# Kernel tuning notes

Hardware: AMD Instinct MI355X
Metric: run time of the kernel (lower is better)

The kernel has to match this reference:

```python
import jax, jax.numpy as jnp
import numpy as np

B, T, C, H = 4, 4096, 384, 64

def setup_inputs() -> dict:
    key = jax.random.key(0)
    ks = jax.random.split(key, 7)
    return {
        "x": jax.random.normal(ks[0], (B, T, C), dtype=jnp.float32),
        "Wk": jax.random.normal(ks[1], (H, C), dtype=jnp.float32) * 0.05,
        "bk": jax.random.normal(ks[2], (H,), dtype=jnp.float32) * 0.05,
        "Wq": jax.random.normal(ks[3], (H, C), dtype=jnp.float32) * 0.05,
        "bq": jax.random.normal(ks[4], (H,), dtype=jnp.float32) * 0.05,
        "Wv": jax.random.normal(ks[5], (H, C), dtype=jnp.float32) * 0.05,
        "bv": jax.random.normal(ks[6], (H,), dtype=jnp.float32) * 0.05,
    }

def reference(x, Wk, bk, Wq, bq, Wv, bv):
    # Faithful to the source, including its quirks:
    #   - q = self.value(x)   (query uses the VALUE projection; Wq/bq unused)
    #   - scale = C ** -0.5 with C = embedding dim (384), not head dim
    #   - dropout in eval mode (identity)
    Bb, Tt, Cc = x.shape
    k = x @ Wk.T + bk                                  # (B,T,H)
    q = x @ Wv.T + bv                                  # (B,T,H)  <- bug reproduced
    scale = jnp.float32(Cc) ** -0.5
    scores = jnp.einsum('bth,bsh->bts', q, k) * scale  # (B,T,T)
    mask = jnp.tril(jnp.ones((Tt, Tt), dtype=bool))    # causal mask
    scores = jnp.where(mask, scores, jnp.float32(-jnp.inf))
    w = jax.nn.softmax(scores, axis=-1)                # (B,T,T)
    v = x @ Wv.T + bv                                  # (B,T,H)
    return jnp.einsum('bts,bsh->bth', w, v)            # (B,T,H)
```

## Files before the change

kernel.cpp:

```cpp
#include <hip/hip_runtime.h>

#define T_SEQ 4096
#define CDIM 384

typedef __attribute__((ext_vector_type(8))) short short8;
typedef __attribute__((ext_vector_type(4))) short short4e;
typedef __attribute__((ext_vector_type(4))) float float4e;

#define KSCALE 0.05103103630798288f
#define KE (KSCALE * 1.4426950408889634f)

__device__ inline unsigned short f2bf(float f) {
  unsigned u = __builtin_bit_cast(unsigned, f);
  u += 0x7FFFu + ((u >> 16) & 1u);
  return (unsigned short)(u >> 16);
}

__device__ inline void dma16(const void* g, void* l) {
  __builtin_amdgcn_global_load_lds(
      (const __attribute__((address_space(1))) unsigned int*)g,
      (__attribute__((address_space(3))) unsigned int*)l, 16, 0, 0);
}

__global__ __launch_bounds__(256) void proj_kernel(
    const float* __restrict__ x, const float* __restrict__ Wk, const float* __restrict__ bk,
    const float* __restrict__ Wv, const float* __restrict__ bv,
    unsigned short* __restrict__ Ktil, unsigned short* __restrict__ Qrow,
    unsigned short* __restrict__ Vtil) {
  __shared__ alignas(16) char plds[24576];
  unsigned short (*Wl)[5120] = (unsigned short (*)[5120])plds;
  const int tid = threadIdx.x;
  const int lane = tid & 63;
  const int w = tid >> 6;
  const int lid = lane & 15, quad = lane >> 4;
  const int blockRow0 = blockIdx.x * 64;
  const float* xr = x + (size_t)(blockRow0 + w * 16 + lid) * CDIM;

  float4e wreg[4];
  int wcol[4], wpart[4];
#pragma unroll
  for (int i = 0; i < 4; i++) {
    const int f = tid + 256 * i;
    wcol[i] = f >> 3; wpart[i] = f & 7;
  }
  auto wload = [&](int kc) {
#pragma unroll
    for (int i = 0; i < 4; i++) {
      const float* wsrc = (wcol[i] < 64)
          ? (Wk + (size_t)wcol[i] * CDIM + kc * 32 + wpart[i] * 4)
          : (Wv + (size_t)(wcol[i] - 64) * CDIM + kc * 32 + wpart[i] * 4);
      wreg[i] = *(const float4e*)wsrc;
    }
  };
  auto wstage = [&](int bufi) {
#pragma unroll
    for (int i = 0; i < 4; i++) {
      short4e s;
#pragma unroll
      for (int jj = 0; jj < 4; jj++) s[jj] = (short)f2bf(wreg[i][jj]);
      *(short4e*)(&Wl[bufi][wcol[i] * 40 + wpart[i] * 4]) = s;
    }
  };
  float4e xa0[2], xa1[2];
  auto xload = [&](int kc, int slot) {
    xa0[slot] = *(const float4e*)(xr + kc * 32 + quad * 8);
    xa1[slot] = *(const float4e*)(xr + kc * 32 + quad * 8 + 4);
  };

  wload(0); wstage(0);
  wload(1);
  xload(0, 0); xload(1, 1);
  __syncthreads();

  float4e acc[8];
#pragma unroll
  for (int n = 0; n < 8; n++) acc[n] = (float4e){0.f, 0.f, 0.f, 0.f};

  for (int kc = 0; kc < 12; kc++) {
    if (kc < 11) wstage((kc + 1) & 1);
    if (kc < 10) wload(kc + 2);
    const int slot = kc & 1;
    short8 af;
#pragma unroll
    for (int jj = 0; jj < 4; jj++) {
      af[jj] = (short)f2bf(xa0[slot][jj]);
      af[4 + jj] = (short)f2bf(xa1[slot][jj]);
    }
    if (kc < 10) xload(kc + 2, slot);
#pragma unroll
    for (int n = 0; n < 8; n++) {
      short8 bf = *(const short8*)(&Wl[kc & 1][(n * 16 + lid) * 40 + quad * 8]);
      acc[n] = __builtin_amdgcn_mfma_f32_16x16x32_bf16(af, bf, acc[n], 0, 0, 0);
    }
    __syncthreads();
  }

  unsigned short* Sl = (unsigned short*)plds;
  const int b = blockRow0 >> 12;
  const int kt32 = (blockRow0 & 4095) >> 5;
  const int sec = w >> 1;
  const int kob = (w & 1) * 16 + quad * 4;
#pragma unroll
  for (int n = 0; n < 8; n++) {
    const int col = n * 16 + lid;
    const float bias = (n < 4) ? bk[col] : bv[col - 64];
#pragma unroll
    for (int i = 0; i < 4; i++) {
      const int ko = kob + i;
      const float val = acc[n][i] + bias;
      if (n < 4) {
        Sl[sec * 6144 + ko * 64 + (((col >> 3) ^ (ko & 7)) * 8) + (col & 7)] = f2bf(val);
      } else {
        const int hh = col - 64;
        Sl[sec * 6144 + 4096 + ko * 64 + hh] = f2bf(val * KE);
        Sl[sec * 6144 + 2048 + hh * 32 + (((ko >> 3) ^ ((hh >> 1) & 3)) * 8) + (ko & 7)] = f2bf(val);
      }
    }
  }
  __syncthreads();
#pragma unroll
  for (int s = 0; s < 2; s++) {
    const size_t tile = (size_t)(b * 128 + kt32 + s) * 2048;
    *(short8*)(Ktil + tile + tid * 8) = *(const short8*)(&Sl[s * 6144 + tid * 8]);
    *(short8*)(Vtil + tile + tid * 8) = *(const short8*)(&Sl[s * 6144 + 2048 + tid * 8]);
  }
#pragma unroll
  for (int r = 0; r < 2; r++) {
    const int slot = tid + r * 256;
    const int s2 = slot >> 8, off = slot & 255;
    *(short8*)(Qrow + (size_t)blockRow0 * 64 + slot * 8) =
        *(const short8*)(&Sl[s2 * 6144 + 4096 + off * 8]);
  }
}

__global__ __launch_bounds__(256, 2) void attn_kernel(
    const unsigned short* __restrict__ Ktil, const unsigned short* __restrict__ Qrow,
    const unsigned short* __restrict__ Vtil,
    float* __restrict__ Opart, float* __restrict__ MLpart,
    int segT, int maxseg, int segshift) {
  __shared__ alignas(16) char lds[51200];
  const int j = blockIdx.x;
  const int b = j & 3;
  const int rest = j >> 2;
  const int qb = 31 - (rest >> segshift);
  const int seg = rest & (maxseg - 1);
  const int t0 = seg * segT;
  const int tendb = 2 * qb + 2;
  if (t0 >= tendb) return;
  const int tend = (t0 + segT < tendb) ? t0 + segT : tendb;

  const int wv = threadIdx.x >> 6;
  const int lane = threadIdx.x & 63;
  const int lid = lane & 15, quad = lane >> 4;
  const int qt = qb * 4 + wv;
  const int q0 = qt * 32;
  const int tcap = qt >> 1;

  const unsigned short* Qb = Qrow + (size_t)(b * T_SEQ + q0) * 64;
  const char* Kg = (const char*)(Ktil + (size_t)(b * 128) * 2048);
  const char* Vg = (const char*)(Vtil + (size_t)(b * 128) * 2048);
  char* Pbase = lds + 32768 + wv * 4608;

  short8 Qf[2][2];
#pragma unroll
  for (int qq = 0; qq < 2; qq++)
#pragma unroll
    for (int h = 0; h < 2; h++)
      Qf[qq][h] = *(const short8*)(Qb + (size_t)(qq * 16 + lid) * 64 + h * 32 + quad * 8);

  float4e Ot[2][4];
  float lrow[2] = {0.f, 0.f};
#pragma unroll
  for (int qq = 0; qq < 2; qq++)
#pragma unroll
    for (int cc = 0; cc < 4; cc++) Ot[qq][cc] = (float4e){0.f, 0.f, 0.f, 0.f};
  const float4e zero4 = (float4e){0.f, 0.f, 0.f, 0.f};

  auto stage = [&](int t, int bufi) {
#pragma unroll
    for (int c = 0; c < 4; c++) {
      const int o = wv * 4 + c;
      const char* src = (o < 8) ? (Kg + (size_t)t * 8192 + o * 1024)
                                : (Vg + (size_t)t * 8192 + (o - 8) * 1024);
      char* dst = (o < 8) ? (lds + bufi * 8192 + o * 1024)
                          : (lds + 16384 + bufi * 8192 + (o - 8) * 1024);
      dma16(src + lane * 16, dst);
    }
  };

  stage(t0, 0);
  __asm__ __volatile__("s_waitcnt vmcnt(0)" ::: "memory");
  __syncthreads();

  for (int t = t0; t < tend; t++) {
    const int cb = (t - t0) & 1, nb = cb ^ 1;
    if (t + 1 < tend) stage(t + 1, nb);

    if (t <= tcap) {
      const int k0 = t * 64;
#pragma unroll
      for (int ksub = 0; ksub < 2; ksub++) {
        short8 Kf[2][2];
#pragma unroll
        for (int kb2 = 0; kb2 < 2; kb2++) {
          const int row32 = kb2 * 16 + lid;
#pragma unroll
          for (int h = 0; h < 2; h++) {
            const int gran = (h * 4 + quad) ^ (row32 & 7);
            Kf[kb2][h] = *(const short8*)(lds + cb * 8192 + ksub * 4096 + row32 * 128 + gran * 16);
          }
        }
        float4e St[2][2];
#pragma unroll
        for (int qq = 0; qq < 2; qq++)
#pragma unroll
          for (int kb2 = 0; kb2 < 2; kb2++) {
            float4e s = __builtin_amdgcn_mfma_f32_16x16x32_bf16(Kf[kb2][0], Qf[qq][0], zero4, 0, 0, 0);
            St[qq][kb2] = __builtin_amdgcn_mfma_f32_16x16x32_bf16(Kf[kb2][1], Qf[qq][1], s, 0, 0, 0);
          }
        const int k0s = k0 + ksub * 32;
#pragma unroll
        for (int qq = 0; qq < 2; qq++) {
          const int qg = q0 + qq * 16 + lid;
          if (k0s + 31 > q0 + qq * 16) {
#pragma unroll
            for (int kb2 = 0; kb2 < 2; kb2++) {
              const int kbase = k0s + kb2 * 16 + quad * 4;
#pragma unroll
              for (int i = 0; i < 4; i++)
                if (kbase + i > qg) St[qq][kb2][i] = -__builtin_inff();
            }
          }
#pragma unroll
          for (int kb2 = 0; kb2 < 2; kb2++) {
            float p0 = __builtin_amdgcn_exp2f(fminf(St[qq][kb2][0], 80.f));
            float p1 = __builtin_amdgcn_exp2f(fminf(St[qq][kb2][1], 80.f));
            float p2 = __builtin_amdgcn_exp2f(fminf(St[qq][kb2][2], 80.f));
            float p3 = __builtin_amdgcn_exp2f(fminf(St[qq][kb2][3], 80.f));
            lrow[qq] += (p0 + p1) + (p2 + p3);
            unsigned d0 = __builtin_amdgcn_perm(__builtin_bit_cast(unsigned, p1),
                                                __builtin_bit_cast(unsigned, p0), 0x07060302u);
            unsigned d1 = __builtin_amdgcn_perm(__builtin_bit_cast(unsigned, p3),
                                                __builtin_bit_cast(unsigned, p2), 0x07060302u);
            uint2 dd = {d0, d1};
            *(uint2*)(Pbase + qq * 2304 + lid * 144 + ksub * 64 + kb2 * 32 + quad * 8) = dd;
          }
        }
      }
      __builtin_amdgcn_wave_barrier();
      __asm__ __volatile__("s_waitcnt lgkmcnt(0)" ::: "memory");
      short8 Pf[2][2];
#pragma unroll
      for (int qq = 0; qq < 2; qq++)
#pragma unroll
        for (int ksub = 0; ksub < 2; ksub++)
          Pf[qq][ksub] = *(const short8*)(Pbase + qq * 2304 + lid * 144 + ksub * 64 + quad * 16);
#pragma unroll
      for (int ksub = 0; ksub < 2; ksub++) {
        short8 Vf[4];
#pragma unroll
        for (int cc = 0; cc < 4; cc++) {
          const int hh = cc * 16 + lid;
          const int gran = quad ^ ((hh >> 1) & 3);
          Vf[cc] = *(const short8*)(lds + 16384 + cb * 8192 + ksub * 4096 + hh * 64 + gran * 16);
        }
#pragma unroll
        for (int qq = 0; qq < 2; qq++)
#pragma unroll
          for (int cc = 0; cc < 4; cc++)
            Ot[qq][cc] = __builtin_amdgcn_mfma_f32_16x16x32_bf16(Vf[cc], Pf[qq][ksub], Ot[qq][cc], 0, 0, 0);
      }
      __builtin_amdgcn_wave_barrier();
    }

    __asm__ __volatile__("s_waitcnt vmcnt(0)" ::: "memory");
    __syncthreads();
  }

  float lsum[2];
#pragma unroll
  for (int qq = 0; qq < 2; qq++) {
    float ss = lrow[qq];
    ss += __shfl_xor(ss, 16);
    ss += __shfl_xor(ss, 32);
    lsum[qq] = ss;
  }
  const size_t pidx = (size_t)(b * 128 + qt) * maxseg + seg;
  float* Ob = Opart + pidx * 2048;
#pragma unroll
  for (int qq = 0; qq < 2; qq++)
#pragma unroll
    for (int cc = 0; cc < 4; cc++)
      *(float4e*)(Ob + (size_t)(qq * 16 + lid) * 64 + cc * 16 + quad * 4) = Ot[qq][cc];
  float* ml = MLpart + pidx * 64;
  if (quad == 0) {
#pragma unroll
    for (int qq = 0; qq < 2; qq++) ml[32 + qq * 16 + lid] = lsum[qq];
  }
}

__global__ __launch_bounds__(256) void combine_kernel(
    const float* __restrict__ Opart, const float* __restrict__ MLpart,
    float* __restrict__ out, int st2, int maxseg) {
  const int bq = blockIdx.x;
  const int qt = bq & 127;
  const int nseg = ((qt >> 1) >> st2) + 1;
  const int tid = threadIdx.x;
  __shared__ float sInv[32];
  const float* ml = MLpart + (size_t)bq * maxseg * 64;
  if (tid < 32) {
    float den = 0.f;
    for (int s = 0; s < nseg; s++) den += ml[s * 64 + 32 + tid];
    sInv[tid] = 1.0f / den;
  }
  __syncthreads();
  const float4e* Ob4 = (const float4e*)(Opart + (size_t)bq * maxseg * 2048);
  float4e* out4 = (float4e*)(out + (size_t)bq * 2048);
#pragma unroll
  for (int idx = tid; idx < 512; idx += 256) {
    float4e a = (float4e){0.f, 0.f, 0.f, 0.f};
    for (int s = 0; s < nseg; s++) {
      float4e v = Ob4[s * 512 + idx];
#pragma unroll
      for (int jj = 0; jj < 4; jj++) a[jj] += v[jj];
    }
    const float inv = sInv[idx >> 4];
#pragma unroll
    for (int jj = 0; jj < 4; jj++) a[jj] *= inv;
    out4[idx] = a;
  }
}

extern "C" void kernel_launch(void* const* d_in, const int* in_sizes, int n_in,
                              void* d_out, int out_size, void* d_ws, size_t ws_size,
                              hipStream_t stream) {
  const float* x  = (const float*)d_in[0];
  const float* Wk = (const float*)d_in[1];
  const float* bk = (const float*)d_in[2];
  const float* Wv = (const float*)d_in[5];
  const float* bv = (const float*)d_in[6];
  float* out = (float*)d_out;
  char* ws = (char*)d_ws;

  unsigned short* Ktil = (unsigned short*)(ws);
  unsigned short* Qrow = (unsigned short*)(ws + (2u << 20));
  unsigned short* Vtil = (unsigned short*)(ws + (4u << 20));
  float* Opart = (float*)(ws + (6u << 20));

  int maxseg, segshift, segT, st2;
  if (ws_size >= ((size_t)48 << 20))      { maxseg = 8; segshift = 3; segT = 8;  st2 = 3; }
  else if (ws_size >= ((size_t)24 << 20)) { maxseg = 4; segshift = 2; segT = 16; st2 = 4; }
  else                                    { maxseg = 1; segshift = 0; segT = 64; st2 = 6; }
  float* MLpart = (float*)(ws + (6u << 20) + (size_t)maxseg * 512 * 2048 * 4);

  hipLaunchKernelGGL(proj_kernel, dim3(256), dim3(256), 0, stream,
                     x, Wk, bk, Wv, bv, Ktil, Qrow, Vtil);
  hipLaunchKernelGGL(attn_kernel, dim3(4 * 32 * maxseg), dim3(256), 0, stream,
                     Ktil, Qrow, Vtil, Opart, MLpart, segT, maxseg, segshift);
  hipLaunchKernelGGL(combine_kernel, dim3(512), dim3(256), 0, stream,
                     Opart, MLpart, out, st2, maxseg);
}
```

Baseline: 126.5 us.

## Fuse split-KV combine into attention kernel via atomic last-block reduction

Removes the separate combine kernel. Each attention block writes its partial output and row sums with cache-coherent stores and then increments a per-query-block atomic counter. The last segment to finish sums the partials and writes the normalized output. Query blocks with a single segment write straight to the output. The split is now fixed at four segments of 16 and a memset of the counters is added, which drops the workspace-size-based choice of eight segments and adds serialized reduction tail work in the last block.

```diff
diff --git a/kernel.cpp b/kernel.cpp
--- a/kernel.cpp
+++ b/kernel.cpp
@@ -6,6 +6,7 @@
 typedef __attribute__((ext_vector_type(8))) short short8;
 typedef __attribute__((ext_vector_type(4))) short short4e;
 typedef __attribute__((ext_vector_type(4))) float float4e;
+typedef __attribute__((ext_vector_type(4))) unsigned int uint4e;
 
 #define KSCALE 0.05103103630798288f
 #define KE (KSCALE * 1.4426950408889634f)
@@ -20,6 +21,25 @@
   __builtin_amdgcn_global_load_lds(
       (const __attribute__((address_space(1))) unsigned int*)g,
       (__attribute__((address_space(3))) unsigned int*)l, 16, 0, 0);
+}
+
+__device__ inline void gstore16_cc(void* p, uint4e v) {
+  asm volatile("global_store_dwordx4 %0, %1, off sc0 sc1" :: "v"(p), "v"(v) : "memory");
+}
+__device__ inline void gstore4_cc(void* p, float v) {
+  asm volatile("global_store_dword %0, %1, off sc0 sc1" :: "v"(p), "v"(v) : "memory");
+}
+__device__ inline float4e gload16_cc(const void* p) {
+  uint4e r;
+  asm volatile("global_load_dwordx4 %0, %1, off sc0 sc1\n\ts_waitcnt vmcnt(0)"
+               : "=v"(r) : "v"(p) : "memory");
+  return __builtin_bit_cast(float4e, r);
+}
+__device__ inline float gload4_cc(const void* p) {
+  float r;
+  asm volatile("global_load_dword %0, %1, off sc0 sc1\n\ts_waitcnt vmcnt(0)"
+               : "=v"(r) : "v"(p) : "memory");
+  return r;
 }
 
 __global__ __launch_bounds__(256) void proj_kernel(
@@ -137,20 +157,22 @@
     const unsigned short* __restrict__ Ktil, const unsigned short* __restrict__ Qrow,
     const unsigned short* __restrict__ Vtil,
     float* __restrict__ Opart, float* __restrict__ MLpart,
-    int segT, int maxseg, int segshift) {
+    int* __restrict__ cnt, float* __restrict__ out) {
   __shared__ alignas(16) char lds[51200];
   const int j = blockIdx.x;
   const int b = j & 3;
   const int rest = j >> 2;
-  const int qb = 31 - (rest >> segshift);
-  const int seg = rest & (maxseg - 1);
-  const int t0 = seg * segT;
+  const int qb = 31 - (rest >> 2);
+  const int seg = rest & 3;
+  const int t0 = seg * 16;
   const int tendb = 2 * qb + 2;
   if (t0 >= tendb) return;
-  const int tend = (t0 + segT < tendb) ? t0 + segT : tendb;
+  const int tend = (t0 + 16 < tendb) ? t0 + 16 : tendb;
+  const int nseg = (tendb + 15) >> 4;
 
   const int wv = threadIdx.x >> 6;
-  const int lane = threadIdx.x & 63;
+  const int tid = threadIdx.x;
+  const int lane = tid & 63;
   const int lid = lane & 15, quad = lane >> 4;
   const int qt = qb * 4 + wv;
   const int q0 = qt * 32;
@@ -285,49 +307,73 @@
     ss += __shfl_xor(ss, 32);
     lsum[qq] = ss;
   }
-  const size_t pidx = (size_t)(b * 128 + qt) * maxseg + seg;
+
+  if (nseg == 1) {
+    float* ob = out + (size_t)(b * T_SEQ + q0) * 64;
+#pragma unroll
+    for (int qq = 0; qq < 2; qq++) {
+      const float inv = 1.0f / lsum[qq];
+#pragma unroll
+      for (int cc = 0; cc < 4; cc++) {
+        float4e v = Ot[qq][cc];
+#pragma unroll
+        for (int jj = 0; jj < 4; jj++) v[jj] *= inv;
+        *(float4e*)(ob + (size_t)(qq * 16 + lid) * 64 + cc * 16 + quad * 4) = v;
+      }
+    }
+    return;
+  }
+
+  const size_t pidx = (size_t)(b * 128 + qt) * 4 + seg;
   float* Ob = Opart + pidx * 2048;
 #pragma unroll
   for (int qq = 0; qq < 2; qq++)
 #pragma unroll
     for (int cc = 0; cc < 4; cc++)
-      *(float4e*)(Ob + (size_t)(qq * 16 + lid) * 64 + cc * 16 + quad * 4) = Ot[qq][cc];
-  float* ml = MLpart + pidx * 64;
+      gstore16_cc(Ob + (size_t)(qq * 16 + lid) * 64 + cc * 16 + quad * 4,
+                  __builtin_bit_cast(uint4e, Ot[qq][cc]));
   if (quad == 0) {
 #pragma unroll
-    for (int qq = 0; qq < 2; qq++) ml[32 + qq * 16 + lid] = lsum[qq];
-  }
-}
-
-__global__ __launch_bounds__(256) void combine_kernel(
-    const float* __restrict__ Opart, const float* __restrict__ MLpart,
-    float* __restrict__ out, int st2, int maxseg) {
-  const int bq = blockIdx.x;
-  const int qt = bq & 127;
-  const int nseg = ((qt >> 1) >> st2) + 1;
-  const int tid = threadIdx.x;
-  __shared__ float sInv[32];
-  const float* ml = MLpart + (size_t)bq * maxseg * 64;
-  if (tid < 32) {
+    for (int qq = 0; qq < 2; qq++)
+      gstore4_cc(MLpart + pidx * 64 + 32 + qq * 16 + lid, lsum[qq]);
+  }
+  __asm__ __volatile__("s_waitcnt vmcnt(0)" ::: "memory");
+  __syncthreads();
+
+  int* flag = (int*)lds;
+  if (tid == 0) {
+    const int old = atomicAdd(&cnt[b * 32 + qb], 1);
+    flag[0] = (old == nseg - 1) ? 1 : 0;
+  }
+  __syncthreads();
+  if (!flag[0]) return;
+
+  float* sInv = (float*)(lds + 64);
+  if (tid < 128) {
+    const int q4 = tid >> 5, row = tid & 31;
+    const size_t mbase = ((size_t)(b * 128 + qb * 4 + q4) * 4) * 64;
     float den = 0.f;
-    for (int s = 0; s < nseg; s++) den += ml[s * 64 + 32 + tid];
+    for (int s = 0; s < nseg; s++) den += gload4_cc(MLpart + mbase + s * 64 + 32 + row);
     sInv[tid] = 1.0f / den;
   }
   __syncthreads();
-  const float4e* Ob4 = (const float4e*)(Opart + (size_t)bq * maxseg * 2048);
-  float4e* out4 = (float4e*)(out + (size_t)bq * 2048);
-#pragma unroll
-  for (int idx = tid; idx < 512; idx += 256) {
+  const float4e* Op4 = (const float4e*)Opart;
+  float4e* out4 = (float4e*)out;
+#pragma unroll
+  for (int it = 0; it < 8; it++) {
+    const int idx = tid + it * 256;
+    const int q4 = idx >> 9, off = idx & 511;
+    const size_t pb = ((size_t)(b * 128 + qb * 4 + q4) * 4) * 512;
     float4e a = (float4e){0.f, 0.f, 0.f, 0.f};
     for (int s = 0; s < nseg; s++) {
-      float4e v = Ob4[s * 512 + idx];
+      float4e v = gload16_cc(Op4 + pb + s * 512 + off);
 #pragma unroll
       for (int jj = 0; jj < 4; jj++) a[jj] += v[jj];
     }
-    const float inv = sInv[idx >> 4];
+    const float inv = sInv[q4 * 32 + (off >> 4)];
 #pragma unroll
     for (int jj = 0; jj < 4; jj++) a[jj] *= inv;
-    out4[idx] = a;
+    out4[(size_t)(b * T_SEQ + (qb * 4 + q4) * 32) * 16 + off] = a;
   }
 }
 
@@ -346,17 +392,12 @@
   unsigned short* Qrow = (unsigned short*)(ws + (2u << 20));
   unsigned short* Vtil = (unsigned short*)(ws + (4u << 20));
   float* Opart = (float*)(ws + (6u << 20));
-
-  int maxseg, segshift, segT, st2;
-  if (ws_size >= ((size_t)48 << 20))      { maxseg = 8; segshift = 3; segT = 8;  st2 = 3; }
-  else if (ws_size >= ((size_t)24 << 20)) { maxseg = 4; segshift = 2; segT = 16; st2 = 4; }
-  else                                    { maxseg = 1; segshift = 0; segT = 64; st2 = 6; }
-  float* MLpart = (float*)(ws + (6u << 20) + (size_t)maxseg * 512 * 2048 * 4);
-
+  float* MLpart = (float*)(ws + (23u << 20));
+  int* cnt = (int*)(ws + (23u << 20) + (600u << 10));
+
+  hipMemsetAsync(cnt, 0, 512, stream);
   hipLaunchKernelGGL(proj_kernel, dim3(256), dim3(256), 0, stream,
                      x, Wk, bk, Wv, bv, Ktil, Qrow, Vtil);
-  hipLaunchKernelGGL(attn_kernel, dim3(4 * 32 * maxseg), dim3(256), 0, stream,
-                     Ktil, Qrow, Vtil, Opart, MLpart, segT, maxseg, segshift);
-  hipLaunchKernelGGL(combine_kernel, dim3(512), dim3(256), 0, stream,
-                     Opart, MLpart, out, st2, maxseg);
-}
+  hipLaunchKernelGGL(attn_kernel, dim3(512), dim3(256), 0, stream,
+                     Ktil, Qrow, Vtil, Opart, MLpart, cnt, out);
+}
```

Result: no change. 125.7 us (-0.6%).

## Shuffle P through ds_bpermute instead of LDS staging and raise occupancy

Applied to the files above, without the earlier changes.

The softmax probabilities P are no longer written to a per-wave LDS scratch area and read back. Each wave now rearranges them into the MFMA B-operand layout with ds_bpermute lane shuffles and issues the PV MFMAs right after each 32-key sub-tile. This drops the 18 KB P buffer, shrinking LDS to 32 KB, and launch bounds are raised to 4 blocks per CU for more occupancy. In exchange the register budget tightens, which risks spills, and the MLpart offset is now fixed while the mid-size workspace configuration is removed.

```diff
diff --git a/kernel.cpp b/kernel.cpp
--- a/kernel.cpp
+++ b/kernel.cpp
@@ -133,12 +133,12 @@
   }
 }
 
-__global__ __launch_bounds__(256, 2) void attn_kernel(
+__global__ __launch_bounds__(256, 4) void attn_kernel(
     const unsigned short* __restrict__ Ktil, const unsigned short* __restrict__ Qrow,
     const unsigned short* __restrict__ Vtil,
     float* __restrict__ Opart, float* __restrict__ MLpart,
     int segT, int maxseg, int segshift) {
-  __shared__ alignas(16) char lds[51200];
+  __shared__ alignas(16) char lds[32768];
   const int j = blockIdx.x;
   const int b = j & 3;
   const int rest = j >> 2;
@@ -159,7 +159,6 @@
   const unsigned short* Qb = Qrow + (size_t)(b * T_SEQ + q0) * 64;
   const char* Kg = (const char*)(Ktil + (size_t)(b * 128) * 2048);
   const char* Vg = (const char*)(Vtil + (size_t)(b * 128) * 2048);
-  char* Pbase = lds + 32768 + wv * 4608;
 
   short8 Qf[2][2];
 #pragma unroll
@@ -175,6 +174,10 @@
 #pragma unroll
     for (int cc = 0; cc < 4; cc++) Ot[qq][cc] = (float4e){0.f, 0.f, 0.f, 0.f};
   const float4e zero4 = (float4e){0.f, 0.f, 0.f, 0.f};
+
+  const int idxA = ((((quad * 2) & 3) * 16 + lid) * 4);
+  const int idxB = ((((quad * 2 + 1) & 3) * 16 + lid) * 4);
+  const bool hiHalf = (quad >= 2);
 
   auto stage = [&](int t, int bufi) {
 #pragma unroll
@@ -218,6 +221,13 @@
             float4e s = __builtin_amdgcn_mfma_f32_16x16x32_bf16(Kf[kb2][0], Qf[qq][0], zero4, 0, 0, 0);
             St[qq][kb2] = __builtin_amdgcn_mfma_f32_16x16x32_bf16(Kf[kb2][1], Qf[qq][1], s, 0, 0, 0);
           }
+        short8 Vf[4];
+#pragma unroll
+        for (int cc = 0; cc < 4; cc++) {
+          const int hh = cc * 16 + lid;
+          const int gran = quad ^ ((hh >> 1) & 3);
+          Vf[cc] = *(const short8*)(lds + 16384 + cb * 8192 + ksub * 4096 + hh * 64 + gran * 16);
+        }
         const int k0s = k0 + ksub * 32;
 #pragma unroll
         for (int qq = 0; qq < 2; qq++) {
@@ -231,6 +241,7 @@
                 if (kbase + i > qg) St[qq][kb2][i] = -__builtin_inff();
             }
           }
+          unsigned d[2][2];
 #pragma unroll
           for (int kb2 = 0; kb2 < 2; kb2++) {
             float p0 = __builtin_amdgcn_exp2f(fminf(St[qq][kb2][0], 80.f));
@@ -238,39 +249,35 @@
             float p2 = __builtin_amdgcn_exp2f(fminf(St[qq][kb2][2], 80.f));
             float p3 = __builtin_amdgcn_exp2f(fminf(St[qq][kb2][3], 80.f));
             lrow[qq] += (p0 + p1) + (p2 + p3);
-            unsigned d0 = __builtin_amdgcn_perm(__builtin_bit_cast(unsigned, p1),
-                                                __builtin_bit_cast(unsigned, p0), 0x07060302u);
-            unsigned d1 = __builtin_amdgcn_perm(__builtin_bit_cast(unsigned, p3),
-                                                __builtin_bit_cast(unsigned, p2), 0x07060302u);
-            uint2 dd = {d0, d1};
-            *(uint2*)(Pbase + qq * 2304 + lid * 144 + ksub * 64 + kb2 * 32 + quad * 8) = dd;
-          }
+            d[kb2][0] = __builtin_amdgcn_perm(__builtin_bit_cast(unsigned, p1),
+                                              __builtin_bit_cast(unsigned, p0), 0x07060302u);
+            d[kb2][1] = __builtin_amdgcn_perm(__builtin_bit_cast(unsigned, p3),
+                                              __builtin_bit_cast(unsigned, p2), 0x07060302u);
+          }
+          unsigned w0a = __builtin_amdgcn_ds_bpermute(idxA, (int)d[0][0]);
+          unsigned w1a = __builtin_amdgcn_ds_bpermute(idxA, (int)d[0][1]);
+          unsigned w2a = __builtin_amdgcn_ds_bpermute(idxB, (int)d[0][0]);
+          unsigned w3a = __builtin_amdgcn_ds_bpermute(idxB, (int)d[0][1]);
+          unsigned w0b = __builtin_amdgcn_ds_bpermute(idxA, (int)d[1][0]);
+          unsigned w1b = __builtin_amdgcn_ds_bpermute(idxA, (int)d[1][1]);
+          unsigned w2b = __builtin_amdgcn_ds_bpermute(idxB, (int)d[1][0]);
+          unsigned w3b = __builtin_amdgcn_ds_bpermute(idxB, (int)d[1][1]);
+          unsigned pw[4];
+          pw[0] = hiHalf ? w0b : w0a;
+          pw[1] = hiHalf ? w1b : w1a;
+          pw[2] = hiHalf ? w2b : w2a;
+          pw[3] = hiHalf ? w3b : w3a;
+          short8 Pf;
+#pragma unroll
+          for (int dw = 0; dw < 4; dw++) {
+            Pf[dw * 2]     = (short)(pw[dw] & 0xFFFFu);
+            Pf[dw * 2 + 1] = (short)(pw[dw] >> 16);
+          }
+#pragma unroll
+          for (int cc = 0; cc < 4; cc++)
+            Ot[qq][cc] = __builtin_amdgcn_mfma_f32_16x16x32_bf16(Vf[cc], Pf, Ot[qq][cc], 0, 0, 0);
         }
       }
-      __builtin_amdgcn_wave_barrier();
-      __asm__ __volatile__("s_waitcnt lgkmcnt(0)" ::: "memory");
-      short8 Pf[2][2];
-#pragma unroll
-      for (int qq = 0; qq < 2; qq++)
-#pragma unroll
-        for (int ksub = 0; ksub < 2; ksub++)
-          Pf[qq][ksub] = *(const short8*)(Pbase + qq * 2304 + lid * 144 + ksub * 64 + quad * 16);
-#pragma unroll
-      for (int ksub = 0; ksub < 2; ksub++) {
-        short8 Vf[4];
-#pragma unroll
-        for (int cc = 0; cc < 4; cc++) {
-          const int hh = cc * 16 + lid;
-          const int gran = quad ^ ((hh >> 1) & 3);
-          Vf[cc] = *(const short8*)(lds + 16384 + cb * 8192 + ksub * 4096 + hh * 64 + gran * 16);
-        }
-#pragma unroll
-        for (int qq = 0; qq < 2; qq++)
-#pragma unroll
-          for (int cc = 0; cc < 4; cc++)
-            Ot[qq][cc] = __builtin_amdgcn_mfma_f32_16x16x32_bf16(Vf[cc], Pf[qq][ksub], Ot[qq][cc], 0, 0, 0);
-      }
-      __builtin_amdgcn_wave_barrier();
     }
 
     __asm__ __volatile__("s_waitcnt vmcnt(0)" ::: "memory");
@@ -346,12 +353,11 @@
   unsigned short* Qrow = (unsigned short*)(ws + (2u << 20));
   unsigned short* Vtil = (unsigned short*)(ws + (4u << 20));
   float* Opart = (float*)(ws + (6u << 20));
+  float* MLpart = (float*)(ws + (40u << 20));
 
   int maxseg, segshift, segT, st2;
-  if (ws_size >= ((size_t)48 << 20))      { maxseg = 8; segshift = 3; segT = 8;  st2 = 3; }
-  else if (ws_size >= ((size_t)24 << 20)) { maxseg = 4; segshift = 2; segT = 16; st2 = 4; }
-  else                                    { maxseg = 1; segshift = 0; segT = 64; st2 = 6; }
-  float* MLpart = (float*)(ws + (6u << 20) + (size_t)maxseg * 512 * 2048 * 4);
+  if (ws_size >= ((size_t)48 << 20)) { maxseg = 8; segshift = 3; segT = 8;  st2 = 3; }
+  else                               { maxseg = 1; segshift = 0; segT = 64; st2 = 6; }
 
   hipLaunchKernelGGL(proj_kernel, dim3(256), dim3(256), 0, stream,
                      x, Wk, bk, Wv, bv, Ktil, Qrow, Vtil);
```

After: 127.7 us. Within noise of the previous version (+1.0%).
